# Kernel optimization log

Measured on AMD Instinct MI355X. Metric: run time of the kernel, lower is better.

The kernel has to match this reference:

```python
import jax, jax.numpy as jnp
import numpy as np

EMBED_DIM = 768
N_HEADS = 12
HEAD_DIM = EMBED_DIM // N_HEADS


def setup_inputs() -> dict:
    key = jax.random.key(0)
    ks = jax.random.split(key, 5)
    B, T, C = 2, 4096, EMBED_DIM
    x = jax.random.normal(ks[0], (B, T, C), dtype=jnp.float32)
    # nn.Linear default init scale ~ 1/sqrt(fan_in); use small-scale normals
    s = 1.0 / np.sqrt(C)
    W_qkv = jax.random.normal(ks[1], (C, 3 * C), dtype=jnp.float32) * s
    b_qkv = jax.random.normal(ks[2], (3 * C,), dtype=jnp.float32) * s
    W_proj = jax.random.normal(ks[3], (C, C), dtype=jnp.float32) * s
    b_proj = jax.random.normal(ks[4], (C,), dtype=jnp.float32) * s
    return {"x": x, "W_qkv": W_qkv, "b_qkv": b_qkv, "W_proj": W_proj, "b_proj": b_proj}


def reference(x, W_qkv, b_qkv, W_proj, b_proj):
    B, T, C = x.shape
    H, D = N_HEADS, HEAD_DIM
    qkv = x @ W_qkv + b_qkv                      # [B,T,3C]
    q, k, v = jnp.split(qkv, 3, axis=2)
    # [B,T,C] -> [B,H,T,D]
    q = q.reshape(B, T, H, D).transpose(0, 2, 1, 3)
    k = k.reshape(B, T, H, D).transpose(0, 2, 1, 3)
    v = v.reshape(B, T, H, D).transpose(0, 2, 1, 3)
    scale = 1.0 / jnp.sqrt(jnp.float32(D)).astype(x.dtype)
    attn = jnp.einsum('bhtd,bhsd->bhts', q, k) * scale   # [B,H,T,T]
    causal = jnp.tril(jnp.ones((T, T), dtype=bool))
    attn = jnp.where(causal, attn, jnp.float32(-jnp.inf).astype(attn.dtype))
    attn = jax.nn.softmax(attn, axis=-1)
    # dropout p=0.0 -> identity
    out = jnp.einsum('bhts,bhsd->bhtd', attn, v)          # [B,H,T,D]
    out = out.transpose(0, 2, 1, 3).reshape(B, T, C)
    return out @ W_proj + b_proj
```

## Files before the change

kernel.cpp:

```cpp
#include <hip/hip_runtime.h>
#include <math.h>

#define T_SEQ 4096
#define CDIM  768
#define NH    12
#define HD    64
#define BATCH 2
#define MROWS (BATCH * T_SEQ)
#define N3C   (3 * CDIM)
#define HEADS_TOTAL (BATCH * NH)
#define QKV_ELEMS   ((size_t)HEADS_TOTAL * T_SEQ * HD)

#define QSCALE 0.18033688011112042f
#define SSHIFT -12.0f

typedef __bf16 bf16x8 __attribute__((ext_vector_type(8)));
typedef __bf16 bf16x4 __attribute__((ext_vector_type(4)));
typedef __bf16 bf16x2 __attribute__((ext_vector_type(2)));
typedef float  f32x4  __attribute__((ext_vector_type(4)));
typedef short  s16x4  __attribute__((ext_vector_type(4)));

union b4u { bf16x4 h; s16x4 s; };
__device__ __forceinline__ s16x4 as_s16(bf16x4 v) { b4u u; u.h = v; return u.s; }

typedef __attribute__((address_space(1))) const void as1_cvoid;
typedef __attribute__((address_space(3))) void as3_void;

__device__ __forceinline__ void gl16(const void* g, void* l) {
  __builtin_amdgcn_global_load_lds((as1_cvoid*)g, (as3_void*)l, 16, 0, 0);
}

__global__ __launch_bounds__(256) void cast_x_kernel(
    const float* __restrict__ x, __bf16* __restrict__ xb) {
  int i = (blockIdx.x * 256 + threadIdx.x) * 8;
  float4 a = *(const float4*)&x[i];
  float4 b = *(const float4*)&x[i + 4];
  bf16x8 o;
  o[0] = (__bf16)a.x; o[1] = (__bf16)a.y; o[2] = (__bf16)a.z; o[3] = (__bf16)a.w;
  o[4] = (__bf16)b.x; o[5] = (__bf16)b.y; o[6] = (__bf16)b.z; o[7] = (__bf16)b.w;
  *(bf16x8*)&xb[i] = o;
}

__global__ __launch_bounds__(256) void tcast_kernel(
    const float* __restrict__ W, __bf16* __restrict__ Wt, int K, int N) {
  __shared__ float tile[64][65];
  const int t  = threadIdx.x;
  const int k0 = blockIdx.y * 64, n0 = blockIdx.x * 64;
  const int r  = t >> 4, c4 = (t & 15) << 2;
#pragma unroll
  for (int i = 0; i < 4; ++i) {
    float4 v = *(const float4*)&W[(size_t)(k0 + r + i * 16) * N + n0 + c4];
    tile[r + i * 16][c4 + 0] = v.x; tile[r + i * 16][c4 + 1] = v.y;
    tile[r + i * 16][c4 + 2] = v.z; tile[r + i * 16][c4 + 3] = v.w;
  }
  __syncthreads();
#pragma unroll
  for (int i = 0; i < 4; ++i) {
    int nr = r + i * 16;
    bf16x4 o;
    o[0] = (__bf16)tile[c4 + 0][nr]; o[1] = (__bf16)tile[c4 + 1][nr];
    o[2] = (__bf16)tile[c4 + 2][nr]; o[3] = (__bf16)tile[c4 + 3][nr];
    *(bf16x4*)&Wt[(size_t)(n0 + nr) * K + k0 + c4] = o;
  }
}

__device__ __forceinline__ void mm_loop(const __bf16* __restrict__ A,
                                        const __bf16* __restrict__ Bt,
                                        int m0, int n0, __bf16* smem,
                                        f32x4 acc[4][4]) {
  const int t = threadIdx.x, wv = t >> 6, lane = t & 63;
  const int g2 = lane >> 4, c = lane & 15;
  __bf16* At = smem;
  __bf16* Bs = smem + 4096;
  const int ch0 = wv * 64 + lane;
  const int ch1 = 256 + ch0;
  const __bf16* gA0 = A  + (size_t)(m0 + (ch0 >> 2)) * CDIM + ((ch0 & 3) << 3);
  const __bf16* gA1 = A  + (size_t)(m0 + (ch1 >> 2)) * CDIM + ((ch1 & 3) << 3);
  const __bf16* gB0 = Bt + (size_t)(n0 + (ch0 >> 2)) * CDIM + ((ch0 & 3) << 3);
  const __bf16* gB1 = Bt + (size_t)(n0 + (ch1 >> 2)) * CDIM + ((ch1 & 3) << 3);
  __bf16* lA0 = At + (size_t)(wv * 64) * 8;
  __bf16* lA1 = At + (size_t)(256 + wv * 64) * 8;
  __bf16* lB0 = Bs + (size_t)(wv * 64) * 8;
  __bf16* lB1 = Bs + (size_t)(256 + wv * 64) * 8;
  const int mw = (wv & 1) << 6, nw = (wv >> 1) << 6;

  for (int kk = 0; kk < CDIM / 32; ++kk) {
    __syncthreads();
    gl16(gA0, lA0); gl16(gA1, lA1);
    gl16(gB0, lB0); gl16(gB1, lB1);
    gA0 += 32; gA1 += 32; gB0 += 32; gB1 += 32;
    __syncthreads();
    bf16x8 af[4], bfr[4];
#pragma unroll
    for (int mq = 0; mq < 4; ++mq)
      af[mq] = *(const bf16x8*)&At[(size_t)(mw + mq * 16 + c) * 32 + (g2 << 3)];
#pragma unroll
    for (int nq = 0; nq < 4; ++nq)
      bfr[nq] = *(const bf16x8*)&Bs[(size_t)(nw + nq * 16 + c) * 32 + (g2 << 3)];
#pragma unroll
    for (int mq = 0; mq < 4; ++mq)
#pragma unroll
      for (int nq = 0; nq < 4; ++nq)
        acc[mq][nq] = __builtin_amdgcn_mfma_f32_16x16x32_bf16(
            af[mq], bfr[nq], acc[mq][nq], 0, 0, 0);
  }
  __syncthreads();
}

__global__ __launch_bounds__(256) void qkv_mm_kernel(
    const __bf16* __restrict__ xb, const __bf16* __restrict__ Wt,
    const float* __restrict__ bias, __bf16* __restrict__ Qw,
    __bf16* __restrict__ Kw, __bf16* __restrict__ Vtw) {
  __shared__ __align__(16) __bf16 smem[18432];
  f32x4 acc[4][4];
#pragma unroll
  for (int i = 0; i < 4; ++i)
#pragma unroll
    for (int j = 0; j < 4; ++j) acc[i][j] = (f32x4){0.f, 0.f, 0.f, 0.f};

  const int m0 = blockIdx.y * 128, n0 = blockIdx.x * 128;
  mm_loop(xb, Wt, m0, n0, smem, acc);

  const int t = threadIdx.x, wv = t >> 6, lane = t & 63;
  const int g2 = lane >> 4, c = lane & 15;
  const int sel = n0 / CDIM;
  const int nn0 = n0 - sel * CDIM;
  const int h   = (nn0 >> 6) + (wv >> 1);
  const int mbase = m0 + ((wv & 1) << 6);
  const int b = mbase >> 12, tp0 = mbase & 4095;
  const int bh = b * NH + h;
  __bf16* Ep = smem + wv * 4608;
  float bcol[4];
#pragma unroll
  for (int nq = 0; nq < 4; ++nq)
    bcol[nq] = bias[n0 + ((wv >> 1) << 6) + nq * 16 + c];

  const int r8 = lane >> 3, c8 = (lane & 7) << 3;
  if (sel < 2) {
    const float scl = (sel == 0) ? QSCALE : 1.0f;
#pragma unroll
    for (int mq = 0; mq < 4; ++mq)
#pragma unroll
      for (int nq = 0; nq < 4; ++nq)
#pragma unroll
        for (int r = 0; r < 4; ++r)
          Ep[(size_t)(mq * 16 + (g2 << 2) + r) * 72 + nq * 16 + c] =
              (__bf16)((acc[mq][nq][r] + bcol[nq]) * scl);
    asm volatile("s_waitcnt lgkmcnt(0)" ::: "memory");
    __bf16* dst = (sel == 0) ? Qw : Kw;
#pragma unroll
    for (int p = 0; p < 8; ++p) {
      int row = p * 8 + r8;
      bf16x8 v = *(const bf16x8*)&Ep[(size_t)row * 72 + c8];
      *(bf16x8*)&dst[((size_t)bh * T_SEQ + tp0 + row) * HD + c8] = v;
    }
  } else {
#pragma unroll
    for (int mq = 0; mq < 4; ++mq)
#pragma unroll
      for (int nq = 0; nq < 4; ++nq)
#pragma unroll
        for (int r = 0; r < 4; ++r)
          Ep[(size_t)(nq * 16 + c) * 72 + mq * 16 + (g2 << 2) + r] =
              (__bf16)(acc[mq][nq][r] + bcol[nq]);
    asm volatile("s_waitcnt lgkmcnt(0)" ::: "memory");
#pragma unroll
    for (int p = 0; p < 8; ++p) {
      int d = p * 8 + r8;
      bf16x8 v = *(const bf16x8*)&Ep[(size_t)d * 72 + c8];
      *(bf16x8*)&Vtw[((size_t)bh * HD + d) * T_SEQ + tp0 + c8] = v;
    }
  }
}

__device__ __forceinline__ void stage_tile(const __bf16* gk, const __bf16* gv,
                                           __bf16* ldsK, __bf16* ldsV) {
  gl16(gk,              ldsK);
  gl16(gk + 8 * HD,     ldsK + 8 * 64);
  gl16(gv,              ldsV);
  gl16(gv + 8 * T_SEQ,  ldsV + 8 * 64);
}

__device__ __forceinline__ void attn_tile(
    const __bf16* __restrict__ Qb, const __bf16* __restrict__ Kb,
    const __bf16* __restrict__ Vb, __bf16* __restrict__ O,
    int b, int hh, int qt, int wv, int lane, int g2, int c,
    __bf16 (*KT)[64][64], __bf16 (*VT)[64][64]) {
  const int qw = qt * 64 + wv * 16;

  bf16x8 qf0 = *(const bf16x8*)&Qb[(size_t)(qw + c) * HD +      (g2 << 3)];
  bf16x8 qf1 = *(const bf16x8*)&Qb[(size_t)(qw + c) * HD + 32 + (g2 << 3)];

  f32x4 ot[4];
#pragma unroll
  for (int dt = 0; dt < 4; ++dt) ot[dt] = (f32x4){0.f, 0.f, 0.f, 0.f};
  f32x4 lacc = (f32x4){0.f, 0.f, 0.f, 0.f};

  const int rr = lane >> 3;
  const int lc = ((lane & 7) ^ rr) << 3;
  const __bf16* gk = Kb + (size_t)(wv * 16 + rr) * HD    + lc;
  const __bf16* gv = Vb + (size_t)(wv * 16 + rr) * T_SEQ + lc;

  stage_tile(gk, gv, &KT[0][wv * 16][0], &VT[0][wv * 16][0]);
  gk += 64 * HD; gv += 64;
  __syncthreads();

  const int swz  = (c & 7) << 3;
  const int qloc = (wv << 4) + c;
  const f32x4 SINIT = (f32x4){SSHIFT, SSHIFT, SSHIFT, SSHIFT};

#pragma unroll 1
  for (int kt = 0; kt <= qt; ++kt) {
    const int cur = kt & 1;
    if (kt < qt) {
      stage_tile(gk, gv, &KT[cur ^ 1][wv * 16][0], &VT[cur ^ 1][wv * 16][0]);
      gk += 64 * HD; gv += 64;
    }

    f32x4 S[4];
#pragma unroll
    for (int st = 0; st < 4; ++st) {
      bf16x8 kfa = *(const bf16x8*)&KT[cur][st * 16 + c][(g2 << 3) ^ swz];
      bf16x8 kfb = *(const bf16x8*)&KT[cur][st * 16 + c][((4 + g2) << 3) ^ swz];
      S[st] = __builtin_amdgcn_mfma_f32_16x16x32_bf16(kfa, qf0, SINIT, 0, 0, 0);
      S[st] = __builtin_amdgcn_mfma_f32_16x16x32_bf16(kfb, qf1, S[st], 0, 0, 0);
    }

    if (kt == qt) {
#pragma unroll
      for (int st = 0; st < 4; ++st)
#pragma unroll
        for (int r = 0; r < 4; ++r)
          if ((st << 4) + (g2 << 2) + r > qloc) S[st][r] = -INFINITY;
    }

    s16x4 pf[4];
#pragma unroll
    for (int st = 0; st < 4; ++st) {
      bf16x4 ph;
#pragma unroll
      for (int r = 0; r < 4; ++r) {
        float pl = __builtin_amdgcn_exp2f(S[st][r]);
        lacc[r] += pl;
        ph[r] = (__bf16)pl;
      }
      pf[st] = as_s16(ph);
    }

#pragma unroll
    for (int dt = 0; dt < 4; ++dt) {
#pragma unroll
      for (int st = 0; st < 4; ++st) {
        bf16x4 vh = *(const bf16x4*)&VT[cur][dt * 16 + c]
                                       [((st << 4) + (g2 << 2)) ^ swz];
        ot[dt] = __builtin_amdgcn_mfma_f32_16x16x16bf16_1k(as_s16(vh), pf[st],
                                                           ot[dt], 0, 0, 0);
      }
    }
    __syncthreads();
  }

  float l = lacc[0] + lacc[1] + lacc[2] + lacc[3];
  l += __shfl_xor(l, 16);
  l += __shfl_xor(l, 32);
  const float inv = 1.f / l;
  __bf16* orow = O + ((size_t)(b * T_SEQ + qw + c)) * CDIM + hh * HD;
#pragma unroll
  for (int dt = 0; dt < 4; ++dt) {
    bf16x4 v;
    v[0] = (__bf16)(ot[dt][0] * inv); v[1] = (__bf16)(ot[dt][1] * inv);
    v[2] = (__bf16)(ot[dt][2] * inv); v[3] = (__bf16)(ot[dt][3] * inv);
    *(bf16x4*)&orow[dt * 16 + (g2 << 2)] = v;
  }
}

__global__ __launch_bounds__(256) void attn_kernel(
    const __bf16* __restrict__ Q, const __bf16* __restrict__ K,
    const __bf16* __restrict__ Vt, __bf16* __restrict__ O) {
  __shared__ __align__(16) __bf16 KT[2][64][64];
  __shared__ __align__(16) __bf16 VT[2][64][64];

  const int t    = threadIdx.x;
  const int wv   = t >> 6;
  const int lane = t & 63;
  const int g2   = lane >> 4;
  const int c    = lane & 15;
  const int bh   = blockIdx.x;
  const int p    = (int)blockIdx.y;

  const __bf16* Qb = Q  + (size_t)bh * T_SEQ * HD;
  const __bf16* Kb = K  + (size_t)bh * T_SEQ * HD;
  const __bf16* Vb = Vt + (size_t)bh * HD * T_SEQ;
  const int b = bh / NH, hh = bh % NH;

  attn_tile(Qb, Kb, Vb, O, b, hh, p,      wv, lane, g2, c, KT, VT);
  attn_tile(Qb, Kb, Vb, O, b, hh, 63 - p, wv, lane, g2, c, KT, VT);
}

__global__ __launch_bounds__(256) void proj_mm_kernel(
    const __bf16* __restrict__ Ob, const __bf16* __restrict__ Wt,
    const float* __restrict__ bias, float* __restrict__ out) {
  __shared__ __align__(16) __bf16 smem[8192];
  f32x4 acc[4][4];
#pragma unroll
  for (int i = 0; i < 4; ++i)
#pragma unroll
    for (int j = 0; j < 4; ++j) acc[i][j] = (f32x4){0.f, 0.f, 0.f, 0.f};

  const int m0 = blockIdx.y * 128, n0 = blockIdx.x * 128;
  mm_loop(Ob, Wt, m0, n0, smem, acc);

  const int t = threadIdx.x, wv = t >> 6, lane = t & 63;
  const int g2 = lane >> 4, c = lane & 15;
  const int mb = m0 + ((wv & 1) << 6), nb = n0 + ((wv >> 1) << 6);
  float bcol[4];
#pragma unroll
  for (int nq = 0; nq < 4; ++nq) bcol[nq] = bias[nb + nq * 16 + c];
#pragma unroll
  for (int mq = 0; mq < 4; ++mq)
#pragma unroll
    for (int nq = 0; nq < 4; ++nq)
#pragma unroll
      for (int r = 0; r < 4; ++r)
        out[(size_t)(mb + mq * 16 + (g2 << 2) + r) * CDIM + nb + nq * 16 + c] =
            acc[mq][nq][r] + bcol[nq];
}

extern "C" void kernel_launch(void* const* d_in, const int* in_sizes, int n_in,
                              void* d_out, int out_size, void* d_ws, size_t ws_size,
                              hipStream_t stream) {
  (void)in_sizes; (void)n_in; (void)out_size; (void)ws_size;
  const float* x      = (const float*)d_in[0];
  const float* W_qkv  = (const float*)d_in[1];
  const float* b_qkv  = (const float*)d_in[2];
  const float* W_proj = (const float*)d_in[3];
  const float* b_proj = (const float*)d_in[4];
  float* out = (float*)d_out;

  __bf16* Qw     = (__bf16*)d_ws;
  __bf16* Kw     = Qw  + QKV_ELEMS;
  __bf16* Vtw    = Kw  + QKV_ELEMS;
  __bf16* Ob     = Vtw + QKV_ELEMS;
  __bf16* xb     = Ob  + QKV_ELEMS;
  __bf16* Wqkvt  = xb  + QKV_ELEMS;
  __bf16* Wprojt = Wqkvt + (size_t)CDIM * N3C;

  cast_x_kernel<<<MROWS * CDIM / 2048, 256, 0, stream>>>(x, xb);
  tcast_kernel<<<dim3(N3C / 64, CDIM / 64), 256, 0, stream>>>(
      W_qkv, Wqkvt, CDIM, N3C);
  tcast_kernel<<<dim3(CDIM / 64, CDIM / 64), 256, 0, stream>>>(
      W_proj, Wprojt, CDIM, CDIM);

  qkv_mm_kernel<<<dim3(N3C / 128, MROWS / 128), 256, 0, stream>>>(
      xb, Wqkvt, b_qkv, Qw, Kw, Vtw);

  attn_kernel<<<dim3(HEADS_TOTAL, 32), 256, 0, stream>>>(Qw, Kw, Vtw, Ob);

  proj_mm_kernel<<<dim3(CDIM / 128, MROWS / 128), 256, 0, stream>>>(
      Ob, Wprojt, b_proj, out);
}
```

Measured before the change: 249.4 us.

## Load K fragments directly from global and compute row sums via MFMA

Drops the K shared-memory staging. Each wave now reads its K fragments straight from global memory into registers every iteration, and the LDS ring buffer holds only V. The per-lane exp accumulation and cross-lane shuffles for the softmax denominator are replaced by an extra MFMA against a vector of ones, which sums the bf16-rounded probabilities. The K loads are not prefetched, so global latency sits on the critical path right before the QK MFMAs, and all four waves load the same K tile redundantly.

```diff
diff --git a/kernel.cpp b/kernel.cpp
--- a/kernel.cpp
+++ b/kernel.cpp
@@ -173,19 +173,11 @@
   }
 }
 
-__device__ __forceinline__ void stage_tile(const __bf16* gk, const __bf16* gv,
-                                           __bf16* ldsK, __bf16* ldsV) {
-  gl16(gk,              ldsK);
-  gl16(gk + 8 * HD,     ldsK + 8 * 64);
-  gl16(gv,              ldsV);
-  gl16(gv + 8 * T_SEQ,  ldsV + 8 * 64);
-}
-
 __device__ __forceinline__ void attn_tile(
     const __bf16* __restrict__ Qb, const __bf16* __restrict__ Kb,
     const __bf16* __restrict__ Vb, __bf16* __restrict__ O,
     int b, int hh, int qt, int wv, int lane, int g2, int c,
-    __bf16 (*KT)[64][64], __bf16 (*VT)[64][64]) {
+    __bf16 (*VT)[64][64]) {
   const int qw = qt * 64 + wv * 16;
 
   bf16x8 qf0 = *(const bf16x8*)&Qb[(size_t)(qw + c) * HD +      (g2 << 3)];
@@ -194,15 +186,21 @@
   f32x4 ot[4];
 #pragma unroll
   for (int dt = 0; dt < 4; ++dt) ot[dt] = (f32x4){0.f, 0.f, 0.f, 0.f};
-  f32x4 lacc = (f32x4){0.f, 0.f, 0.f, 0.f};
+  f32x4 lt = (f32x4){0.f, 0.f, 0.f, 0.f};
+
+  const bf16x4 onev = {(__bf16)1.f, (__bf16)1.f, (__bf16)1.f, (__bf16)1.f};
+  const s16x4 ones = as_s16(onev);
 
   const int rr = lane >> 3;
   const int lc = ((lane & 7) ^ rr) << 3;
-  const __bf16* gk = Kb + (size_t)(wv * 16 + rr) * HD    + lc;
   const __bf16* gv = Vb + (size_t)(wv * 16 + rr) * T_SEQ + lc;
 
-  stage_tile(gk, gv, &KT[0][wv * 16][0], &VT[0][wv * 16][0]);
-  gk += 64 * HD; gv += 64;
+  const __bf16* gkA = Kb + (size_t)c * HD + (g2 << 3);
+  const __bf16* gkB = Kb + (size_t)(32 + c) * HD + (g2 << 3);
+
+  gl16(gv,             &VT[0][wv * 16][0]);
+  gl16(gv + 8 * T_SEQ, &VT[0][wv * 16 + 8][0]);
+  gv += 64;
   __syncthreads();
 
   const int swz  = (c & 7) << 3;
@@ -212,19 +210,32 @@
 #pragma unroll 1
   for (int kt = 0; kt <= qt; ++kt) {
     const int cur = kt & 1;
+
+    bf16x8 kf0a = *(const bf16x8*)(gkA);
+    bf16x8 kf0b = *(const bf16x8*)(gkA + 32);
+    bf16x8 kf1a = *(const bf16x8*)(gkA + 1024);
+    bf16x8 kf1b = *(const bf16x8*)(gkA + 1056);
+    bf16x8 kf2a = *(const bf16x8*)(gkB);
+    bf16x8 kf2b = *(const bf16x8*)(gkB + 32);
+    bf16x8 kf3a = *(const bf16x8*)(gkB + 1024);
+    bf16x8 kf3b = *(const bf16x8*)(gkB + 1056);
+    gkA += 64 * HD; gkB += 64 * HD;
+
     if (kt < qt) {
-      stage_tile(gk, gv, &KT[cur ^ 1][wv * 16][0], &VT[cur ^ 1][wv * 16][0]);
-      gk += 64 * HD; gv += 64;
+      gl16(gv,             &VT[cur ^ 1][wv * 16][0]);
+      gl16(gv + 8 * T_SEQ, &VT[cur ^ 1][wv * 16 + 8][0]);
+      gv += 64;
     }
 
     f32x4 S[4];
-#pragma unroll
-    for (int st = 0; st < 4; ++st) {
-      bf16x8 kfa = *(const bf16x8*)&KT[cur][st * 16 + c][(g2 << 3) ^ swz];
-      bf16x8 kfb = *(const bf16x8*)&KT[cur][st * 16 + c][((4 + g2) << 3) ^ swz];
-      S[st] = __builtin_amdgcn_mfma_f32_16x16x32_bf16(kfa, qf0, SINIT, 0, 0, 0);
-      S[st] = __builtin_amdgcn_mfma_f32_16x16x32_bf16(kfb, qf1, S[st], 0, 0, 0);
-    }
+    S[0] = __builtin_amdgcn_mfma_f32_16x16x32_bf16(kf0a, qf0, SINIT, 0, 0, 0);
+    S[0] = __builtin_amdgcn_mfma_f32_16x16x32_bf16(kf0b, qf1, S[0], 0, 0, 0);
+    S[1] = __builtin_amdgcn_mfma_f32_16x16x32_bf16(kf1a, qf0, SINIT, 0, 0, 0);
+    S[1] = __builtin_amdgcn_mfma_f32_16x16x32_bf16(kf1b, qf1, S[1], 0, 0, 0);
+    S[2] = __builtin_amdgcn_mfma_f32_16x16x32_bf16(kf2a, qf0, SINIT, 0, 0, 0);
+    S[2] = __builtin_amdgcn_mfma_f32_16x16x32_bf16(kf2b, qf1, S[2], 0, 0, 0);
+    S[3] = __builtin_amdgcn_mfma_f32_16x16x32_bf16(kf3a, qf0, SINIT, 0, 0, 0);
+    S[3] = __builtin_amdgcn_mfma_f32_16x16x32_bf16(kf3b, qf1, S[3], 0, 0, 0);
 
     if (kt == qt) {
 #pragma unroll
@@ -239,11 +250,8 @@
     for (int st = 0; st < 4; ++st) {
       bf16x4 ph;
 #pragma unroll
-      for (int r = 0; r < 4; ++r) {
-        float pl = __builtin_amdgcn_exp2f(S[st][r]);
-        lacc[r] += pl;
-        ph[r] = (__bf16)pl;
-      }
+      for (int r = 0; r < 4; ++r)
+        ph[r] = (__bf16)__builtin_amdgcn_exp2f(S[st][r]);
       pf[st] = as_s16(ph);
     }
 
@@ -257,13 +265,14 @@
                                                            ot[dt], 0, 0, 0);
       }
     }
+#pragma unroll
+    for (int st = 0; st < 4; ++st)
+      lt = __builtin_amdgcn_mfma_f32_16x16x16bf16_1k(ones, pf[st], lt, 0, 0, 0);
+
     __syncthreads();
   }
 
-  float l = lacc[0] + lacc[1] + lacc[2] + lacc[3];
-  l += __shfl_xor(l, 16);
-  l += __shfl_xor(l, 32);
-  const float inv = 1.f / l;
+  const float inv = 1.f / lt[0];
   __bf16* orow = O + ((size_t)(b * T_SEQ + qw + c)) * CDIM + hh * HD;
 #pragma unroll
   for (int dt = 0; dt < 4; ++dt) {
@@ -277,7 +286,6 @@
 __global__ __launch_bounds__(256) void attn_kernel(
     const __bf16* __restrict__ Q, const __bf16* __restrict__ K,
     const __bf16* __restrict__ Vt, __bf16* __restrict__ O) {
-  __shared__ __align__(16) __bf16 KT[2][64][64];
   __shared__ __align__(16) __bf16 VT[2][64][64];
 
   const int t    = threadIdx.x;
@@ -293,8 +301,8 @@
   const __bf16* Vb = Vt + (size_t)bh * HD * T_SEQ;
   const int b = bh / NH, hh = bh % NH;
 
-  attn_tile(Qb, Kb, Vb, O, b, hh, p,      wv, lane, g2, c, KT, VT);
-  attn_tile(Qb, Kb, Vb, O, b, hh, 63 - p, wv, lane, g2, c, KT, VT);
+  attn_tile(Qb, Kb, Vb, O, b, hh, p,      wv, lane, g2, c, VT);
+  attn_tile(Qb, Kb, Vb, O, b, hh, 63 - p, wv, lane, g2, c, VT);
 }
 
 __global__ __launch_bounds__(256) void proj_mm_kernel(
```

Result: slower. 364.3 us (+46.1%).
